# Kernel optimization log

Hardware: AMD Instinct MI355X
Metric: run time of the kernel (lower is better)

The kernel has to match this reference:

```python
import jax, jax.numpy as jnp
import numpy as np

DT = 5e-05
NUM_SUBSTEPS = 100
SPRING_Y = 30000.0
DASHPOT_DAMPING = 100.0
DRAG_DAMPING = 1.0
N_VERTICES = 100000
N_SPRINGS = 1000000


def setup_inputs() -> dict:
    key = jax.random.key(0)
    k1, k2, k3, k4 = jax.random.split(key, 4)
    x = jax.random.normal(k1, (N_VERTICES, 3), dtype=jnp.float32)
    x = x.at[:, 2].add(3.0)  # start mostly above the ground plane z=0
    # spring endpoints, guaranteed distinct so rest length / norm is never 0
    idx1 = jax.random.randint(k2, (N_SPRINGS,), 0, N_VERTICES)
    off = jax.random.randint(k3, (N_SPRINGS,), 1, N_VERTICES)
    idx2 = (idx1 + off) % N_VERTICES
    springs = jnp.stack([idx1, idx2], axis=1).astype(jnp.int64)
    # rest lengths = initial spring lengths (realistic: starts near equilibrium)
    rest = jnp.linalg.norm(x[idx2] - x[idx1], axis=1).astype(jnp.float32)
    masses = jax.random.uniform(k4, (N_VERTICES,), jnp.float32, 0.5, 1.5)
    return {
        "init_vertices": x,
        "init_springs": springs,
        "init_rest_lengths": rest,
        "init_masses": masses,
    }


def reference(init_vertices, init_springs, init_rest_lengths, init_masses):
    idx1 = init_springs[:, 0]
    idx2 = init_springs[:, 1]
    masses = init_masses[:, None]                      # [V,1]
    rest = init_rest_lengths[:, None]                  # [S,1]
    gravity = jnp.array([0.0, 0.0, -9.8], dtype=init_vertices.dtype)
    drag = jnp.exp(jnp.asarray(-DT * DRAG_DAMPING, dtype=init_vertices.dtype))

    def substep(carry, _):
        x, v = carry
        dis = x[idx2] - x[idx1]                        # [S,3] gather
        length = jnp.linalg.norm(dis, axis=1, keepdims=True)
        d = dis / length                               # unit spring direction
        spring_f = SPRING_Y * (length / rest - 1.0) * d
        v_rel = jnp.sum((v[idx2] - v[idx1]) * d, axis=1, keepdims=True)
        f_pair = spring_f + DASHPOT_DAMPING * v_rel * d  # fused spring+dashpot
        forces = masses * gravity                      # [V,3]
        forces = forces.at[idx1].add(f_pair)           # scatter-add
        forces = forces.at[idx2].add(-f_pair)
        v = (v + DT * forces / masses) * drag          # explicit Euler + drag
        x = x + DT * v
        x = x.at[:, 2].set(jnp.maximum(x[:, 2], 0.0))  # ground clamp
        v = v.at[:, 2].set(jnp.where(x[:, 2] == 0.0, 0.0, v[:, 2]))
        return (x, v), None

    v0 = jnp.zeros_like(init_vertices)
    (x, v), _ = jax.lax.scan(substep, (init_vertices, v0), None, length=NUM_SUBSTEPS)
    return x
```

## Files before the change

kernel.cpp:

```cpp
#include <hip/hip_runtime.h>
#include <hip/hip_fp16.h>

#define DT 5e-5f
#define SPRING_Y 30000.0f
#define DASHPOT 100.0f
#define DRAG 0.9999500012499792f
#define NSUB 100



__global__ void init_k(const float* __restrict__ x0, float4* __restrict__ xv,
                       int* __restrict__ deg, int nv) {
    int i = blockIdx.x * blockDim.x + threadIdx.x;
    if (i < nv) {
        xv[2 * i]     = make_float4(x0[3 * i], x0[3 * i + 1], x0[3 * i + 2], 0.0f);
        xv[2 * i + 1] = make_float4(0.0f, 0.0f, 0.0f, 0.0f);
        deg[i] = 0;
    }
}

__global__ void count_k(const int2* __restrict__ springs, int* __restrict__ deg,
                        int ns) {
    int s = blockIdx.x * blockDim.x + threadIdx.x;
    if (s >= ns) return;
    int2 p = springs[s];
    atomicAdd(&deg[p.x], 1);
    atomicAdd(&deg[p.y], 1);
}

__global__ void scan1_k(const int* __restrict__ deg, int* __restrict__ rowstart,
                        int* __restrict__ bsum, int nv) {
    __shared__ int sh[256];
    int t = threadIdx.x;
    int i = blockIdx.x * 256 + t;
    int v = (i < nv) ? deg[i] : 0;
    sh[t] = v;
    __syncthreads();
    for (int off = 1; off < 256; off <<= 1) {
        int add = (t >= off) ? sh[t - off] : 0;
        __syncthreads();
        sh[t] += add;
        __syncthreads();
    }
    if (i < nv) rowstart[i] = sh[t] - v;
    if (t == 255) bsum[blockIdx.x] = sh[255];
}

__global__ void scan2_k(int* __restrict__ bsum, int nb) {
    if (blockIdx.x == 0 && threadIdx.x == 0) {
        int run = 0;
        for (int i = 0; i < nb; ++i) { int x = bsum[i]; bsum[i] = run; run += x; }
    }
}

__global__ void scan3_k(int* __restrict__ rowstart, const int* __restrict__ bsum,
                        int* __restrict__ cursor, int nv) {
    int i = blockIdx.x * blockDim.x + threadIdx.x;
    if (i < nv) {
        int r = rowstart[i] + bsum[blockIdx.x];
        rowstart[i] = r;
        cursor[i]   = r;
    }
}

__global__ void place_sliced_k(const int2* __restrict__ springs,
                               const float* __restrict__ rest,
                               int* __restrict__ cursor, unsigned* __restrict__ csr,
                               int ns, int nv) {
    int b = blockIdx.x;
    int slice = b & 7;
    int s = (b >> 3) * blockDim.x + threadIdx.x;
    if (s >= ns) return;

    int lo = (int)(((long long)slice * nv) >> 3);
    int hi = (int)(((long long)(slice + 1) * nv) >> 3);

    int2 p = springs[s];
    unsigned h = __half_as_ushort(__float2half(1.0f / rest[s])) & 0x7fffu;
    if (p.x >= lo && p.x < hi)
        csr[atomicAdd(&cursor[p.x], 1)] = ((unsigned)p.y << 15) | h;
    if (p.y >= lo && p.y < hi)
        csr[atomicAdd(&cursor[p.y], 1)] = ((unsigned)p.x << 15) | h;
}


__device__ __forceinline__ void spring_accum(
        int par, unsigned e, float msk, float4 t1, float4 t2,
        const float4& xa, const float4& va,
        float& fx, float& fy, float& fz) {
    float invr = __uint_as_float(((e & 0x7fffu) << 13) + (112u << 23));
    float xbx = par ? t2.x : t1.x;
    float xby = par ? t2.y : t1.y;
    float xbz = par ? t2.z : t1.z;
    float ux  = par ? t1.x : t2.x;
    float uy  = par ? t1.y : t2.y;
    float uz  = par ? t1.z : t2.z;
    float vbx = __shfl_xor(ux, 1);
    float vby = __shfl_xor(uy, 1);
    float vbz = __shfl_xor(uz, 1);

    float dx = xbx - xa.x, dy = xby - xa.y, dz = xbz - xa.z;
    float len = sqrtf(dx * dx + dy * dy + dz * dz);
    float il = 1.0f / len;
    float ddx = dx * il, ddy = dy * il, ddz = dz * il;
    float vrel = (vbx - va.x) * ddx + (vby - va.y) * ddy + (vbz - va.z) * ddz;
    float coef = (SPRING_Y * (len * invr - 1.0f) + DASHPOT * vrel) * msk;
    fx += coef * ddx;
    fy += coef * ddy;
    fz += coef * ddz;
}

__global__ void __launch_bounds__(256) substep_k(
        const float4* __restrict__ xvin, float4* __restrict__ xvout,
        const unsigned* __restrict__ adj, const int* __restrict__ deg,
        const int* __restrict__ rowstart,
        const float* __restrict__ mass, int nv,
        float* __restrict__ out) {
    int gid = blockIdx.x * blockDim.x + threadIdx.x;
    int vid = gid >> 3;
    int sub = gid & 7;
    if (vid >= nv) return;

    float4 xa = xvin[2 * vid];
    float4 va = xvin[2 * vid + 1];
    float m = mass[vid];
    int d  = deg[vid];
    int s0 = rowstart[vid];
    int last = s0 + d - 1;
    int par  = sub & 1;
    int base = sub & ~1;
    int niter = (d > base) ? ((d - base + 7) >> 3) : 0;
    int pf = s0 + base;

    float fx = 0.0f, fy = 0.0f, fz = 0.0f;

    for (int u = 0; u < niter; u += 2) {
        int pb0 = pf + 8 * u;
        int pb1 = pb0 + 8;
        unsigned eA0 = adj[min(pb0,     last)];
        unsigned eB0 = adj[min(pb0 + 1, last)];
        unsigned eA1 = adj[min(pb1,     last)];
        unsigned eB1 = adj[min(pb1 + 1, last)];
        int nA0 = (int)(eA0 >> 15), nB0 = (int)(eB0 >> 15);
        int nA1 = (int)(eA1 >> 15), nB1 = (int)(eB1 >> 15);

        float4 t10 = xvin[2 * nA0 + par];
        float4 t20 = xvin[2 * nB0 + (1 - par)];
        float4 t11 = xvin[2 * nA1 + par];
        float4 t21 = xvin[2 * nB1 + (1 - par)];

        {
            float msk = (pb0 + par <= last) ? 1.0f : 0.0f;
            spring_accum(par, par ? eB0 : eA0, msk, t10, t20, xa, va, fx, fy, fz);
        }
        {
            float msk = (pb1 + par <= last) ? 1.0f : 0.0f;
            spring_accum(par, par ? eB1 : eA1, msk, t11, t21, xa, va, fx, fy, fz);
        }
    }

    fx += __shfl_xor(fx, 1);
    fx += __shfl_xor(fx, 2);
    fx += __shfl_xor(fx, 4);
    fy += __shfl_xor(fy, 1);
    fy += __shfl_xor(fy, 2);
    fy += __shfl_xor(fy, 4);
    fz += __shfl_xor(fz, 1);
    fz += __shfl_xor(fz, 2);
    fz += __shfl_xor(fz, 4);

    if (sub == 0) {
        fz += m * (-9.8f);
        float invm = 1.0f / m;

        va.x = (va.x + DT * fx * invm) * DRAG;
        va.y = (va.y + DT * fy * invm) * DRAG;
        va.z = (va.z + DT * fz * invm) * DRAG;

        xa.x += DT * va.x;
        xa.y += DT * va.y;
        xa.z += DT * va.z;
        xa.z = fmaxf(xa.z, 0.0f);
        if (xa.z == 0.0f) va.z = 0.0f;

        xvout[2 * vid]     = xa;
        xvout[2 * vid + 1] = va;

        if (out) {
            out[3 * vid + 0] = xa.x;
            out[3 * vid + 1] = xa.y;
            out[3 * vid + 2] = xa.z;
        }
    }
}

extern "C" void kernel_launch(void* const* d_in, const int* in_sizes, int n_in,
                              void* d_out, int out_size, void* d_ws, size_t ws_size,
                              hipStream_t stream) {
    const float* x0      = (const float*)d_in[0];
    const int2*  springs = (const int2*)d_in[1];
    const float* rest    = (const float*)d_in[2];
    const float* mass    = (const float*)d_in[3];

    const int ns = in_sizes[2];
    const int nv = in_sizes[3];
    const int nb = (nv + 255) / 256;

    char* ws = (char*)d_ws;
    size_t o = 0;
    float4* xva   = (float4*)(ws + o); o += (size_t)nv * 32;
    float4* xvb   = (float4*)(ws + o); o += (size_t)nv * 32;
    int* deg      = (int*)(ws + o);    o += (((size_t)nv * 4 + 15) & ~15ull);
    int* rowstart = (int*)(ws + o);    o += (((size_t)nv * 4 + 15) & ~15ull);
    int* cursor   = (int*)(ws + o);    o += (((size_t)nv * 4 + 15) & ~15ull);
    int* bsum     = (int*)(ws + o);    o += 512 * 4;
    unsigned* csr = (unsigned*)(ws + o);

    dim3 blk(256);
    dim3 vgrid(nb);
    dim3 sgrid((ns + 255) / 256);
    dim3 pgrid(8 * ((ns + 255) / 256));
    dim3 subgrid(((size_t)nv * 8 + 255) / 256);

    init_k<<<vgrid, blk, 0, stream>>>(x0, xva, deg, nv);
    count_k<<<sgrid, blk, 0, stream>>>(springs, deg, ns);
    scan1_k<<<vgrid, blk, 0, stream>>>(deg, rowstart, bsum, nv);
    scan2_k<<<dim3(1), dim3(64), 0, stream>>>(bsum, nb);
    scan3_k<<<vgrid, blk, 0, stream>>>(rowstart, bsum, cursor, nv);
    place_sliced_k<<<pgrid, blk, 0, stream>>>(springs, rest, cursor, csr, ns, nv);

    float4* xi = xva;
    float4* xo = xvb;
    for (int t = 0; t < NSUB; ++t) {
        float* out = (t == NSUB - 1) ? (float*)d_out : nullptr;
        substep_k<<<subgrid, blk, 0, stream>>>(xi, xo, csr, deg, rowstart,
                                               mass, nv, out);
        float4* tmp = xi; xi = xo; xo = tmp;
    }
}
```

Before: 1.869 ms.

## Pack quantized neighbor velocity into position w so gathers read one float4

Measured after the change: 1.967 ms. +5.2%, slower.

```diff
diff --git a/kernel.cpp b/kernel.cpp
--- a/kernel.cpp
+++ b/kernel.cpp
@@ -9,12 +9,37 @@
 
 
 
-__global__ void init_k(const float* __restrict__ x0, float4* __restrict__ xv,
-                       int* __restrict__ deg, int nv) {
+__device__ __forceinline__ float packv(float x, float y, float z) {
+    if (fmaxf(fmaxf(fabsf(x), fabsf(y)), fabsf(z)) > 0.249f)
+        return __uint_as_float(0x80000000u);
+    unsigned qx = (unsigned)(x * 2048.0f + 512.5f);
+    unsigned qy = (unsigned)(y * 2048.0f + 512.5f);
+    unsigned qz = (unsigned)(z * 2048.0f + 512.5f);
+    return __uint_as_float((qx << 20) | (qy << 10) | qz);
+}
+
+__device__ __forceinline__ float3 getvel(float w, const float4* __restrict__ V,
+                                         int n) {
+    unsigned uw = __float_as_uint(w);
+    if (uw & 0x80000000u) {
+        float4 vf = V[n];
+        return make_float3(vf.x, vf.y, vf.z);
+    }
+    float3 v;
+    v.x = (float)((int)((uw >> 20) & 1023u) - 512) * (1.0f / 2048.0f);
+    v.y = (float)((int)((uw >> 10) & 1023u) - 512) * (1.0f / 2048.0f);
+    v.z = (float)((int)( uw        & 1023u) - 512) * (1.0f / 2048.0f);
+    return v;
+}
+
+
+__global__ void init_k(const float* __restrict__ x0, float4* __restrict__ G,
+                       float4* __restrict__ V, int* __restrict__ deg, int nv) {
     int i = blockIdx.x * blockDim.x + threadIdx.x;
     if (i < nv) {
-        xv[2 * i]     = make_float4(x0[3 * i], x0[3 * i + 1], x0[3 * i + 2], 0.0f);
-        xv[2 * i + 1] = make_float4(0.0f, 0.0f, 0.0f, 0.0f);
+        G[i] = make_float4(x0[3 * i], x0[3 * i + 1], x0[3 * i + 2],
+                           packv(0.f, 0.f, 0.f));
+        V[i] = make_float4(0.f, 0.f, 0.f, 0.f);
         deg[i] = 0;
     }
 }
@@ -33,7 +58,7 @@
     __shared__ int sh[256];
     int t = threadIdx.x;
     int i = blockIdx.x * 256 + t;
-    int v = (i < nv) ? deg[i] : 0;
+    int v = (i < nv) ? ((deg[i] + 15) & ~15) : 0;
     sh[t] = v;
     __syncthreads();
     for (int off = 1; off < 256; off <<= 1) {
@@ -47,19 +72,29 @@
 }
 
 __global__ void scan2_k(int* __restrict__ bsum, int nb) {
-    if (blockIdx.x == 0 && threadIdx.x == 0) {
-        int run = 0;
-        for (int i = 0; i < nb; ++i) { int x = bsum[i]; bsum[i] = run; run += x; }
-    }
+    __shared__ int sh[512];
+    int t = threadIdx.x;
+    int v = (t < nb) ? bsum[t] : 0;
+    sh[t] = v;
+    __syncthreads();
+    for (int off = 1; off < 512; off <<= 1) {
+        int add = (t >= off) ? sh[t - off] : 0;
+        __syncthreads();
+        sh[t] += add;
+        __syncthreads();
+    }
+    if (t < nb) bsum[t] = sh[t] - v;
 }
 
 __global__ void scan3_k(int* __restrict__ rowstart, const int* __restrict__ bsum,
-                        int* __restrict__ cursor, int nv) {
+                        const int* __restrict__ deg, int* __restrict__ cursor,
+                        int2* __restrict__ meta, int nv) {
     int i = blockIdx.x * blockDim.x + threadIdx.x;
     if (i < nv) {
         int r = rowstart[i] + bsum[blockIdx.x];
         rowstart[i] = r;
         cursor[i]   = r;
+        meta[i]     = make_int2(r, deg[i]);
     }
 }
 
@@ -83,27 +118,26 @@
         csr[atomicAdd(&cursor[p.y], 1)] = ((unsigned)p.x << 15) | h;
 }
 
-
-__device__ __forceinline__ void spring_accum(
-        int par, unsigned e, float msk, float4 t1, float4 t2,
-        const float4& xa, const float4& va,
+__global__ void pad_k(const int2* __restrict__ meta, unsigned* __restrict__ csr,
+                      int nv) {
+    int v = blockIdx.x * blockDim.x + threadIdx.x;
+    if (v >= nv) return;
+    int2 md = meta[v];
+    if (md.y > 0 && (md.y & 1)) csr[md.x + md.y] = csr[md.x];
+}
+
+
+__device__ __forceinline__ void accum(
+        unsigned e, float4 g, const float4* __restrict__ Vin, float msk,
+        const float4& ga, const float3& va,
         float& fx, float& fy, float& fz) {
     float invr = __uint_as_float(((e & 0x7fffu) << 13) + (112u << 23));
-    float xbx = par ? t2.x : t1.x;
-    float xby = par ? t2.y : t1.y;
-    float xbz = par ? t2.z : t1.z;
-    float ux  = par ? t1.x : t2.x;
-    float uy  = par ? t1.y : t2.y;
-    float uz  = par ? t1.z : t2.z;
-    float vbx = __shfl_xor(ux, 1);
-    float vby = __shfl_xor(uy, 1);
-    float vbz = __shfl_xor(uz, 1);
-
-    float dx = xbx - xa.x, dy = xby - xa.y, dz = xbz - xa.z;
+    float dx = g.x - ga.x, dy = g.y - ga.y, dz = g.z - ga.z;
+    float3 vb = getvel(g.w, Vin, (int)(e >> 15));
     float len = sqrtf(dx * dx + dy * dy + dz * dz);
     float il = 1.0f / len;
     float ddx = dx * il, ddy = dy * il, ddz = dz * il;
-    float vrel = (vbx - va.x) * ddx + (vby - va.y) * ddy + (vbz - va.z) * ddz;
+    float vrel = (vb.x - va.x) * ddx + (vb.y - va.y) * ddy + (vb.z - va.z) * ddz;
     float coef = (SPRING_Y * (len * invr - 1.0f) + DASHPOT * vrel) * msk;
     fx += coef * ddx;
     fy += coef * ddy;
@@ -111,9 +145,9 @@
 }
 
 __global__ void __launch_bounds__(256) substep_k(
-        const float4* __restrict__ xvin, float4* __restrict__ xvout,
-        const unsigned* __restrict__ adj, const int* __restrict__ deg,
-        const int* __restrict__ rowstart,
+        const float4* __restrict__ Gin, float4* __restrict__ Gout,
+        const float4* __restrict__ Vin, float4* __restrict__ Vout,
+        const unsigned* __restrict__ csr, const int2* __restrict__ meta,
         const float* __restrict__ mass, int nv,
         float* __restrict__ out) {
     int gid = blockIdx.x * blockDim.x + threadIdx.x;
@@ -121,42 +155,22 @@
     int sub = gid & 7;
     if (vid >= nv) return;
 
-    float4 xa = xvin[2 * vid];
-    float4 va = xvin[2 * vid + 1];
-    float m = mass[vid];
-    int d  = deg[vid];
-    int s0 = rowstart[vid];
-    int last = s0 + d - 1;
-    int par  = sub & 1;
-    int base = sub & ~1;
-    int niter = (d > base) ? ((d - base + 7) >> 3) : 0;
-    int pf = s0 + base;
+    int2 md = meta[vid];
+    int d = md.y;
+    float4 ga = Gin[vid];
+    float3 va = getvel(ga.w, Vin, vid);
+    int niter = (d > 2 * sub) ? ((d - 2 * sub + 15) >> 4) : 0;
+    const uint2* ap = (const uint2*)(csr + md.x) + sub;
 
     float fx = 0.0f, fy = 0.0f, fz = 0.0f;
 
-    for (int u = 0; u < niter; u += 2) {
-        int pb0 = pf + 8 * u;
-        int pb1 = pb0 + 8;
-        unsigned eA0 = adj[min(pb0,     last)];
-        unsigned eB0 = adj[min(pb0 + 1, last)];
-        unsigned eA1 = adj[min(pb1,     last)];
-        unsigned eB1 = adj[min(pb1 + 1, last)];
-        int nA0 = (int)(eA0 >> 15), nB0 = (int)(eB0 >> 15);
-        int nA1 = (int)(eA1 >> 15), nB1 = (int)(eB1 >> 15);
-
-        float4 t10 = xvin[2 * nA0 + par];
-        float4 t20 = xvin[2 * nB0 + (1 - par)];
-        float4 t11 = xvin[2 * nA1 + par];
-        float4 t21 = xvin[2 * nB1 + (1 - par)];
-
-        {
-            float msk = (pb0 + par <= last) ? 1.0f : 0.0f;
-            spring_accum(par, par ? eB0 : eA0, msk, t10, t20, xa, va, fx, fy, fz);
-        }
-        {
-            float msk = (pb1 + par <= last) ? 1.0f : 0.0f;
-            spring_accum(par, par ? eB1 : eA1, msk, t11, t21, xa, va, fx, fy, fz);
-        }
+    for (int u = 0; u < niter; ++u) {
+        uint2 q = ap[8 * u];
+        float4 g0 = Gin[(int)(q.x >> 15)];
+        float4 g1 = Gin[(int)(q.y >> 15)];
+        accum(q.x, g0, Vin, 1.0f, ga, va, fx, fy, fz);
+        float msk1 = (16 * u + 2 * sub + 1 < d) ? 1.0f : 0.0f;
+        accum(q.y, g1, Vin, msk1, ga, va, fx, fy, fz);
     }
 
     fx += __shfl_xor(fx, 1);
@@ -170,26 +184,28 @@
     fz += __shfl_xor(fz, 4);
 
     if (sub == 0) {
+        float4 vf = Vin[vid];
+        float m = mass[vid];
         fz += m * (-9.8f);
         float invm = 1.0f / m;
 
-        va.x = (va.x + DT * fx * invm) * DRAG;
-        va.y = (va.y + DT * fy * invm) * DRAG;
-        va.z = (va.z + DT * fz * invm) * DRAG;
-
-        xa.x += DT * va.x;
-        xa.y += DT * va.y;
-        xa.z += DT * va.z;
-        xa.z = fmaxf(xa.z, 0.0f);
-        if (xa.z == 0.0f) va.z = 0.0f;
-
-        xvout[2 * vid]     = xa;
-        xvout[2 * vid + 1] = va;
+        vf.x = (vf.x + DT * fx * invm) * DRAG;
+        vf.y = (vf.y + DT * fy * invm) * DRAG;
+        vf.z = (vf.z + DT * fz * invm) * DRAG;
+
+        float px = ga.x + DT * vf.x;
+        float py = ga.y + DT * vf.y;
+        float pz = ga.z + DT * vf.z;
+        pz = fmaxf(pz, 0.0f);
+        if (pz == 0.0f) vf.z = 0.0f;
+
+        Gout[vid] = make_float4(px, py, pz, packv(vf.x, vf.y, vf.z));
+        Vout[vid] = vf;
 
         if (out) {
-            out[3 * vid + 0] = xa.x;
-            out[3 * vid + 1] = xa.y;
-            out[3 * vid + 2] = xa.z;
+            out[3 * vid + 0] = px;
+            out[3 * vid + 1] = py;
+            out[3 * vid + 2] = pz;
         }
     }
 }
@@ -208,12 +224,16 @@
 
     char* ws = (char*)d_ws;
     size_t o = 0;
-    float4* xva   = (float4*)(ws + o); o += (size_t)nv * 32;
-    float4* xvb   = (float4*)(ws + o); o += (size_t)nv * 32;
+    float4* Ga    = (float4*)(ws + o); o += (size_t)nv * 16;
+    float4* Gb    = (float4*)(ws + o); o += (size_t)nv * 16;
+    float4* Va    = (float4*)(ws + o); o += (size_t)nv * 16;
+    float4* Vb    = (float4*)(ws + o); o += (size_t)nv * 16;
     int* deg      = (int*)(ws + o);    o += (((size_t)nv * 4 + 15) & ~15ull);
     int* rowstart = (int*)(ws + o);    o += (((size_t)nv * 4 + 15) & ~15ull);
     int* cursor   = (int*)(ws + o);    o += (((size_t)nv * 4 + 15) & ~15ull);
+    int2* meta    = (int2*)(ws + o);   o += (size_t)nv * 8;
     int* bsum     = (int*)(ws + o);    o += 512 * 4;
+    o = (o + 63) & ~63ull;
     unsigned* csr = (unsigned*)(ws + o);
 
     dim3 blk(256);
@@ -222,19 +242,21 @@
     dim3 pgrid(8 * ((ns + 255) / 256));
     dim3 subgrid(((size_t)nv * 8 + 255) / 256);
 
-    init_k<<<vgrid, blk, 0, stream>>>(x0, xva, deg, nv);
+    init_k<<<vgrid, blk, 0, stream>>>(x0, Ga, Va, deg, nv);
     count_k<<<sgrid, blk, 0, stream>>>(springs, deg, ns);
     scan1_k<<<vgrid, blk, 0, stream>>>(deg, rowstart, bsum, nv);
-    scan2_k<<<dim3(1), dim3(64), 0, stream>>>(bsum, nb);
-    scan3_k<<<vgrid, blk, 0, stream>>>(rowstart, bsum, cursor, nv);
+    scan2_k<<<dim3(1), dim3(512), 0, stream>>>(bsum, nb);
+    scan3_k<<<vgrid, blk, 0, stream>>>(rowstart, bsum, deg, cursor, meta, nv);
     place_sliced_k<<<pgrid, blk, 0, stream>>>(springs, rest, cursor, csr, ns, nv);
-
-    float4* xi = xva;
-    float4* xo = xvb;
+    pad_k<<<vgrid, blk, 0, stream>>>(meta, csr, nv);
+
+    float4* Gi = Ga; float4* Go = Gb;
+    float4* Vi = Va; float4* Vo = Vb;
     for (int t = 0; t < NSUB; ++t) {
         float* out = (t == NSUB - 1) ? (float*)d_out : nullptr;
-        substep_k<<<subgrid, blk, 0, stream>>>(xi, xo, csr, deg, rowstart,
+        substep_k<<<subgrid, blk, 0, stream>>>(Gi, Go, Vi, Vo, csr, meta,
                                                mass, nv, out);
-        float4* tmp = xi; xi = xo; xo = tmp;
-    }
-}
+        float4* tg = Gi; Gi = Go; Go = tg;
+        float4* tv = Vi; Vi = Vo; Vo = tv;
+    }
+}
```
